# Kernel tuning notes

Measured on AMD Instinct MI355X. Metric: run time of the kernel, lower is better.

The kernel has to match this reference:

```python
import jax, jax.numpy as jnp
import numpy as np

B, D_IN, D_ATT, N_PROTO = 262144, 512, 32, 4
GAMMA = 2.0
SCALE = D_ATT ** -0.5
LN_EPS = 1e-5


def setup_inputs() -> dict:
    key = jax.random.key(0)
    ks = jax.random.split(key, 8)
    return {
        "x": jax.random.normal(ks[0], (B, D_IN), dtype=jnp.float32),
        "minority_prob": jax.random.uniform(ks[1], (B,), dtype=jnp.float32),
        "Wq": jax.random.normal(ks[2], (D_ATT, D_IN), dtype=jnp.float32) * (D_IN ** -0.5),
        "bq": jnp.zeros((D_ATT,), dtype=jnp.float32),
        "proto_keys": jax.random.normal(ks[3], (N_PROTO, D_ATT), dtype=jnp.float32) * 0.02,
        "proto_values": jax.random.normal(ks[4], (N_PROTO, D_ATT), dtype=jnp.float32) * 0.02,
        "proto_importance": jnp.ones((N_PROTO,), dtype=jnp.float32) / N_PROTO,
        "focal_alpha": jnp.array([0.6], dtype=jnp.float32),
        "focal_temp": jnp.array([1.0], dtype=jnp.float32),
        "Wo": jax.random.normal(ks[5], (D_ATT, D_ATT), dtype=jnp.float32) * (D_ATT ** -0.5),
        "bo": jnp.zeros((D_ATT,), dtype=jnp.float32),
        "ln_gamma": jnp.ones((D_ATT,), dtype=jnp.float32),
        "ln_beta": jnp.zeros((D_ATT,), dtype=jnp.float32),
    }


def reference(x, minority_prob, Wq, bq, proto_keys, proto_values,
              proto_importance, focal_alpha, focal_temp, Wo, bo, ln_gamma, ln_beta):
    # query projection: [B, D_ATT]
    q = x @ Wq.T + bq
    # prototype scores: [B, N_PROTO]
    scores = q @ proto_keys.T + proto_importance[None, :]
    # focal modulation (per-sample weight broadcast over prototypes)
    uncertainty = 1.0 - jnp.abs(minority_prob - 0.5) * 2.0
    focal_w = focal_alpha * jnp.power(uncertainty + 1e-8, GAMMA) * focal_temp
    scores = scores * (1.0 + focal_w[:, None])
    # softmax over prototypes (dropout is identity at inference)
    weights = jax.nn.softmax(scores * SCALE, axis=-1)
    # attend prototype values: [B, D_ATT]
    attended = weights @ proto_values
    out = attended @ Wo.T + bo
    # layer norm
    mu = jnp.mean(out, axis=-1, keepdims=True)
    var = jnp.var(out, axis=-1, keepdims=True)
    out = (out - mu) * jax.lax.rsqrt(var + LN_EPS) * ln_gamma + ln_beta
    return out, weights
```

## Files before the change

kernel.cpp:

```cpp
#include <hip/hip_runtime.h>

#define B_TOTAL 262144
#define D_IN 512
#define LN_EPS 1e-5f

typedef __attribute__((ext_vector_type(8))) short short8;
typedef __attribute__((ext_vector_type(4))) float f32x4;

__device__ __forceinline__ unsigned short f2bf_rne(float f) {
    union { float f; unsigned int u; } c; c.f = f;
    unsigned int u = c.u;
    u += 0x7fffu + ((u >> 16) & 1u);
    return (unsigned short)(u >> 16);
}

__device__ __forceinline__ short8 cvt8(f32x4 lo, f32x4 hi) {
    short8 r;
    r[0] = (short)f2bf_rne(lo[0]); r[1] = (short)f2bf_rne(lo[1]);
    r[2] = (short)f2bf_rne(lo[2]); r[3] = (short)f2bf_rne(lo[3]);
    r[4] = (short)f2bf_rne(hi[0]); r[5] = (short)f2bf_rne(hi[1]);
    r[6] = (short)f2bf_rne(hi[2]); r[7] = (short)f2bf_rne(hi[3]);
    return r;
}

__global__ __launch_bounds__(256) void faiia_kernel(
    const float* __restrict__ x,
    const float* __restrict__ mprob,
    const float* __restrict__ Wq,
    const float* __restrict__ bq,
    const float* __restrict__ pk,
    const float* __restrict__ pv,
    const float* __restrict__ imp,
    const float* __restrict__ falpha,
    const float* __restrict__ ftemp,
    const float* __restrict__ Wo,
    const float* __restrict__ bo,
    const float* __restrict__ gamma,
    const float* __restrict__ beta,
    float* __restrict__ out)
{
    __shared__ float lds_q[64][33];
    __shared__ float lds_att[64][33];

    const int tid  = threadIdx.x;
    const int wave = tid >> 6;
    const int lane = tid & 63;
    const int blockBase = blockIdx.x * 64;

    const int m    = lane & 15;
    const int quad = lane >> 4;
    const int row  = blockBase + wave * 16 + m;

    const float* ax  = x  + (size_t)row * D_IN + quad * 8;
    const float* bw0 = Wq + (size_t)m   * D_IN + quad * 8;
    const float* bw1 = bw0 + 16 * D_IN;

    f32x4 acc0 = {0.f, 0.f, 0.f, 0.f};
    f32x4 acc1 = {0.f, 0.f, 0.f, 0.f};
    #pragma unroll
    for (int kk = 0; kk < 16; ++kk) {
        f32x4 a0 = *(const f32x4*)(ax  + kk * 32);
        f32x4 a1 = *(const f32x4*)(ax  + kk * 32 + 4);
        f32x4 p0 = *(const f32x4*)(bw0 + kk * 32);
        f32x4 p1 = *(const f32x4*)(bw0 + kk * 32 + 4);
        f32x4 r0 = *(const f32x4*)(bw1 + kk * 32);
        f32x4 r1 = *(const f32x4*)(bw1 + kk * 32 + 4);
        short8 a  = cvt8(a0, a1);
        short8 b0 = cvt8(p0, p1);
        short8 b1 = cvt8(r0, r1);
        acc0 = __builtin_amdgcn_mfma_f32_16x16x32_bf16(a, b0, acc0, 0, 0, 0);
        acc1 = __builtin_amdgcn_mfma_f32_16x16x32_bf16(a, b1, acc1, 0, 0, 0);
    }

    {
        const float bq0 = bq[m];
        const float bq1 = bq[m + 16];
        #pragma unroll
        for (int r = 0; r < 4; ++r) {
            int s = wave * 16 + quad * 4 + r;
            lds_q[s][m]      = acc0[r] + bq0;
            lds_q[s][m + 16] = acc1[r] + bq1;
        }
    }
    __syncthreads();

    const int sLocal = tid >> 2;
    const int part   = tid & 3;
    const int d0     = part * 8;
    const int sample = blockBase + sLocal;

    float q8[8];
    #pragma unroll
    for (int j = 0; j < 8; ++j) q8[j] = lds_q[sLocal][d0 + j];

    float sc[4];
    #pragma unroll
    for (int p = 0; p < 4; ++p) {
        float s = 0.f;
        #pragma unroll
        for (int j = 0; j < 8; ++j) s += q8[j] * pk[p * 32 + d0 + j];
        s += __shfl_xor(s, 1);
        s += __shfl_xor(s, 2);
        sc[p] = s + imp[p];
    }

    const float prob = mprob[sample];
    const float unc  = 1.f - fabsf(prob - 0.5f) * 2.f;
    const float ue   = unc + 1e-8f;
    const float fw   = falpha[0] * ue * ue * ftemp[0];
    const float SCALE = 0.1767766952966369f;
    const float mult  = (1.f + fw) * SCALE;

    float z[4];
    #pragma unroll
    for (int p = 0; p < 4; ++p) z[p] = sc[p] * mult;
    float zmax = fmaxf(fmaxf(z[0], z[1]), fmaxf(z[2], z[3]));
    float w[4], wsum = 0.f;
    #pragma unroll
    for (int p = 0; p < 4; ++p) { w[p] = expf(z[p] - zmax); wsum += w[p]; }
    const float winv = 1.f / wsum;
    #pragma unroll
    for (int p = 0; p < 4; ++p) w[p] *= winv;

    #pragma unroll
    for (int j = 0; j < 8; ++j) {
        float a = 0.f;
        #pragma unroll
        for (int p = 0; p < 4; ++p) a += w[p] * pv[p * 32 + d0 + j];
        lds_att[sLocal][d0 + j] = a;
    }
    __syncthreads();

    float att[32];
    #pragma unroll
    for (int n = 0; n < 32; ++n) att[n] = lds_att[sLocal][n];

    float o[8];
    #pragma unroll
    for (int jo = 0; jo < 8; ++jo) {
        const int n2 = d0 + jo;
        float s = bo[n2];
        #pragma unroll
        for (int n = 0; n < 32; ++n) s += att[n] * Wo[n2 * 32 + n];
        o[jo] = s;
    }

    float s1 = 0.f, s2 = 0.f;
    #pragma unroll
    for (int jo = 0; jo < 8; ++jo) { s1 += o[jo]; s2 += o[jo] * o[jo]; }
    s1 += __shfl_xor(s1, 1); s1 += __shfl_xor(s1, 2);
    s2 += __shfl_xor(s2, 1); s2 += __shfl_xor(s2, 2);
    const float mu   = s1 * (1.f / 32.f);
    const float var  = s2 * (1.f / 32.f) - mu * mu;
    const float rstd = rsqrtf(var + LN_EPS);

    f32x4 res_lo, res_hi;
    #pragma unroll
    for (int jo = 0; jo < 8; ++jo) {
        const int n2 = d0 + jo;
        float y = (o[jo] - mu) * rstd * gamma[n2] + beta[n2];
        if (jo < 4) res_lo[jo] = y; else res_hi[jo - 4] = y;
    }
    *(f32x4*)(out + (size_t)sample * 32 + d0)     = res_lo;
    *(f32x4*)(out + (size_t)sample * 32 + d0 + 4) = res_hi;

    if (part == 0) {
        f32x4 wres;
        #pragma unroll
        for (int p = 0; p < 4; ++p) wres[p] = w[p];
        *(f32x4*)(out + (size_t)B_TOTAL * 32 + (size_t)sample * 4) = wres;
    }
}

extern "C" void kernel_launch(void* const* d_in, const int* in_sizes, int n_in,
                              void* d_out, int out_size, void* d_ws, size_t ws_size,
                              hipStream_t stream) {
    const float* x      = (const float*)d_in[0];
    const float* mprob  = (const float*)d_in[1];
    const float* Wq     = (const float*)d_in[2];
    const float* bq     = (const float*)d_in[3];
    const float* pk     = (const float*)d_in[4];
    const float* pv     = (const float*)d_in[5];
    const float* imp    = (const float*)d_in[6];
    const float* falpha = (const float*)d_in[7];
    const float* ftemp  = (const float*)d_in[8];
    const float* Wo     = (const float*)d_in[9];
    const float* bo     = (const float*)d_in[10];
    const float* gamma  = (const float*)d_in[11];
    const float* beta   = (const float*)d_in[12];
    float* out = (float*)d_out;

    const int blocks = B_TOTAL / 64;
    faiia_kernel<<<blocks, 256, 0, stream>>>(
        x, mprob, Wq, bq, pk, pv, imp, falpha, ftemp, Wo, bo, gamma, beta, out);
}
```

Measured before the change: 858.2 us.

## Stage Wq as bf16 in LDS and stream x through async LDS ring buffer

Each block converts Wq to bf16 once and stores it in LDS in MFMA-fragment order, replacing the per-wave global reloads and reconversion of Wq in every k-step. Rows of x are streamed with global_load_lds into a 4-slot LDS ring, keeping three stages in flight under hand-written vmcnt waits. The float-to-bf16 conversion now uses the compiler's native __bf16 cast instead of manual bit rounding. The cost is a 64 KB LDS footprint per block, which limits occupancy, plus a block-wide Wq staging prologue.

```diff
diff --git a/kernel.cpp b/kernel.cpp
--- a/kernel.cpp
+++ b/kernel.cpp
@@ -7,21 +7,25 @@
 typedef __attribute__((ext_vector_type(8))) short short8;
 typedef __attribute__((ext_vector_type(4))) float f32x4;
 
-__device__ __forceinline__ unsigned short f2bf_rne(float f) {
-    union { float f; unsigned int u; } c; c.f = f;
-    unsigned int u = c.u;
-    u += 0x7fffu + ((u >> 16) & 1u);
-    return (unsigned short)(u >> 16);
+__device__ __forceinline__ short f2bf(float f) {
+    __bf16 h = (__bf16)f;
+    unsigned short u;
+    __builtin_memcpy(&u, &h, sizeof(u));
+    return (short)u;
 }
 
 __device__ __forceinline__ short8 cvt8(f32x4 lo, f32x4 hi) {
     short8 r;
-    r[0] = (short)f2bf_rne(lo[0]); r[1] = (short)f2bf_rne(lo[1]);
-    r[2] = (short)f2bf_rne(lo[2]); r[3] = (short)f2bf_rne(lo[3]);
-    r[4] = (short)f2bf_rne(hi[0]); r[5] = (short)f2bf_rne(hi[1]);
-    r[6] = (short)f2bf_rne(hi[2]); r[7] = (short)f2bf_rne(hi[3]);
+    r[0] = f2bf(lo[0]); r[1] = f2bf(lo[1]);
+    r[2] = f2bf(lo[2]); r[3] = f2bf(lo[3]);
+    r[4] = f2bf(hi[0]); r[5] = f2bf(hi[1]);
+    r[6] = f2bf(hi[2]); r[7] = f2bf(hi[3]);
     return r;
 }
+
+#define GLL(g, l) __builtin_amdgcn_global_load_lds(                      \
+    (const __attribute__((address_space(1))) void*)(g),                  \
+    (__attribute__((address_space(3))) void*)(l), 16, 0, 0)
 
 __global__ __launch_bounds__(256) void faiia_kernel(
     const float* __restrict__ x,
@@ -39,8 +43,11 @@
     const float* __restrict__ beta,
     float* __restrict__ out)
 {
-    __shared__ float lds_q[64][33];
-    __shared__ float lds_att[64][33];
+    __shared__ __align__(16) char smem[65536];
+    short* wq_lds = (short*)smem;
+    float* xbuf   = (float*)(smem + 32768);
+    float (*lds_q)[33]   = (float(*)[33])(smem + 32768);
+    float (*lds_att)[33] = (float(*)[33])(smem + 32768 + 8448);
 
     const int tid  = threadIdx.x;
     const int wave = tid >> 6;
@@ -49,37 +56,67 @@
 
     const int m    = lane & 15;
     const int quad = lane >> 4;
-    const int row  = blockBase + wave * 16 + m;
-
-    const float* ax  = x  + (size_t)row * D_IN + quad * 8;
-    const float* bw0 = Wq + (size_t)m   * D_IN + quad * 8;
-    const float* bw1 = bw0 + 16 * D_IN;
+
+    const float* xrow = x + (size_t)(blockBase + wave * 16 + m) * D_IN + quad * 8;
+    float* xw = xbuf + wave * 512;
+
+    #pragma unroll
+    for (int t = 0; t < 3; ++t) {
+        float* d = xw + t * 2048;
+        GLL(xrow + t * 32,     d);
+        GLL(xrow + t * 32 + 4, d + 256);
+    }
+
+    #pragma unroll
+    for (int it = 0; it < 8; ++it) {
+        const int id = it * 256 + tid;
+        const int n  = id >> 6;
+        const int c  = id & 63;
+        f32x4 v0 = *(const f32x4*)(Wq + n * 512 + c * 8);
+        f32x4 v1 = *(const f32x4*)(Wq + n * 512 + c * 8 + 4);
+        const int sk = c >> 2, q = c & 3;
+        const int ld = q * 16 + (n & 15);
+        const int a  = n >> 4;
+        *(short8*)(wq_lds + sk * 1024 + a * 512 + ld * 8) = cvt8(v0, v1);
+    }
+    __syncthreads();
+
+    const float* myl = xbuf + wave * 512 + lane * 4;
+    const short* bfr = wq_lds + lane * 8;
 
     f32x4 acc0 = {0.f, 0.f, 0.f, 0.f};
     f32x4 acc1 = {0.f, 0.f, 0.f, 0.f};
     #pragma unroll
-    for (int kk = 0; kk < 16; ++kk) {
-        f32x4 a0 = *(const f32x4*)(ax  + kk * 32);
-        f32x4 a1 = *(const f32x4*)(ax  + kk * 32 + 4);
-        f32x4 p0 = *(const f32x4*)(bw0 + kk * 32);
-        f32x4 p1 = *(const f32x4*)(bw0 + kk * 32 + 4);
-        f32x4 r0 = *(const f32x4*)(bw1 + kk * 32);
-        f32x4 r1 = *(const f32x4*)(bw1 + kk * 32 + 4);
-        short8 a  = cvt8(a0, a1);
-        short8 b0 = cvt8(p0, p1);
-        short8 b1 = cvt8(r0, r1);
+    for (int s = 0; s < 16; ++s) {
+        if (s + 3 < 16) {
+            float* d = xw + ((s + 3) & 3) * 2048;
+            GLL(xrow + (s + 3) * 32,     d);
+            GLL(xrow + (s + 3) * 32 + 4, d + 256);
+        }
+        if      (s <= 12) asm volatile("s_waitcnt vmcnt(6)" ::: "memory");
+        else if (s == 13) asm volatile("s_waitcnt vmcnt(4)" ::: "memory");
+        else if (s == 14) asm volatile("s_waitcnt vmcnt(2)" ::: "memory");
+        else              asm volatile("s_waitcnt vmcnt(0)" ::: "memory");
+
+        f32x4 lo = *(const f32x4*)(myl + (s & 3) * 2048);
+        f32x4 hi = *(const f32x4*)(myl + (s & 3) * 2048 + 256);
+        short8 b0 = *(const short8*)(bfr + s * 1024);
+        short8 b1 = *(const short8*)(bfr + s * 1024 + 512);
+        short8 a  = cvt8(lo, hi);
         acc0 = __builtin_amdgcn_mfma_f32_16x16x32_bf16(a, b0, acc0, 0, 0, 0);
         acc1 = __builtin_amdgcn_mfma_f32_16x16x32_bf16(a, b1, acc1, 0, 0, 0);
     }
+
+    __syncthreads();
 
     {
         const float bq0 = bq[m];
         const float bq1 = bq[m + 16];
         #pragma unroll
         for (int r = 0; r < 4; ++r) {
-            int s = wave * 16 + quad * 4 + r;
-            lds_q[s][m]      = acc0[r] + bq0;
-            lds_q[s][m + 16] = acc1[r] + bq1;
+            int sidx = wave * 16 + quad * 4 + r;
+            lds_q[sidx][m]      = acc0[r] + bq0;
+            lds_q[sidx][m + 16] = acc1[r] + bq1;
         }
     }
     __syncthreads();
```

After: 810.2 us. 5.6% less time.
